# Kernel optimization log

Hardware: AMD Instinct MI355X
Metric: run time of the kernel (lower is better)

The kernel has to match this reference:

```python
import jax, jax.numpy as jnp
import numpy as np

DIM = 1024
HID = 2048
E = 4

def setup_inputs() -> dict:
    key = jax.random.key(0)
    ks = jax.random.split(key, 7)
    s = lambda fan_in: 1.0 / np.sqrt(fan_in)
    x = jax.random.normal(ks[0], (2, 2048, DIM), dtype=jnp.float32)
    W1 = jax.random.uniform(ks[1], (E, DIM, HID), jnp.float32, -s(DIM), s(DIM))
    b1 = jax.random.uniform(ks[2], (E, HID), jnp.float32, -s(DIM), s(DIM))
    W2 = jax.random.uniform(ks[3], (E, HID, DIM), jnp.float32, -s(HID), s(HID))
    b2 = jax.random.uniform(ks[4], (E, DIM), jnp.float32, -s(HID), s(HID))
    Wr = jax.random.uniform(ks[5], (DIM, E), jnp.float32, -s(DIM), s(DIM))
    br = jax.random.uniform(ks[6], (E,), jnp.float32, -s(DIM), s(DIM))
    return {"x": x, "W1": W1, "b1": b1, "W2": W2, "b2": b2, "Wr": Wr, "br": br}

def reference(x, W1, b1, W2, b2, Wr, br):
    # router softmax weights: [B,T,E]
    weights = jax.nn.softmax(x @ Wr + br, axis=-1)
    # all-expert MLP: hidden [B,T,E,H]
    h = jax.nn.gelu(jnp.einsum('btd,edh->bteh', x, W1) + b1, approximate=False)
    # expert outputs [B,T,E,D]
    y = jnp.einsum('bteh,ehd->bted', h, W2) + b2
    # softmax-weighted combine over experts
    return jnp.einsum('bte,bted->btd', weights, y)
```

## Files before the change

### kernel.cpp

```cpp
#include <hip/hip_runtime.h>
#include <hip/hip_bf16.h>
#include <math.h>

#define DIM 1024
#define HID 2048
#define NE  4
#define NT  4096
#define KW  (NE*HID)
#define KSPLIT 2
#define KCH (KW / KSPLIT)

typedef __attribute__((ext_vector_type(8))) short short8;
typedef __attribute__((ext_vector_type(4))) short short4v;
typedef __attribute__((ext_vector_type(4))) float floatx4;


__device__ __forceinline__ void async_cp16(const void* g, void* l) {
  __builtin_amdgcn_global_load_lds(
      (const __attribute__((address_space(1))) void*)g,
      (__attribute__((address_space(3))) void*)l, 16, 0, 0);
}

__device__ __forceinline__ short f2bf(float f) {
  union { float f; unsigned u; } x; x.f = f;
  unsigned r = x.u + 0x7fffu + ((x.u >> 16) & 1u);
  return (short)(r >> 16);
}

__device__ __forceinline__ float gelu_fast(float v) {
  float u = 1.595769122f * (v + 0.044715f * v * v * v);
  return v * __builtin_amdgcn_rcpf(1.0f + __expf(-u));
}

#define VMW(n) asm volatile("s_waitcnt vmcnt(" #n ")" ::: "memory")
#define BAR()  __builtin_amdgcn_s_barrier()

__global__ void router_cvt(const float* __restrict__ x, const float* __restrict__ Wr,
                           const float* __restrict__ br, float* __restrict__ wgt,
                           short* __restrict__ xb) {
  const int wv = threadIdx.x >> 6, lane = threadIdx.x & 63;
  const int t = blockIdx.x * 4 + wv;
  const float* xr = x + (size_t)t * DIM;
  short* xo = xb + (size_t)t * DIM;
  float a0 = 0.f, a1 = 0.f, a2 = 0.f, a3 = 0.f;
  #pragma unroll
  for (int p = 0; p < 4; p++) {
    const int d = p * 256 + lane * 4;
    floatx4 v = *(const floatx4*)&xr[d];
    short4v o;
    #pragma unroll
    for (int j = 0; j < 4; j++) {
      o[j] = f2bf(v[j]);
      floatx4 wr = *(const floatx4*)&Wr[(d + j) * 4];
      a0 += v[j] * wr[0]; a1 += v[j] * wr[1];
      a2 += v[j] * wr[2]; a3 += v[j] * wr[3];
    }
    *(short4v*)&xo[d] = o;
  }
  #pragma unroll
  for (int off = 32; off; off >>= 1) {
    a0 += __shfl_down(a0, off);
    a1 += __shfl_down(a1, off);
    a2 += __shfl_down(a2, off);
    a3 += __shfl_down(a3, off);
  }
  a0 = __shfl(a0, 0); a1 = __shfl(a1, 0); a2 = __shfl(a2, 0); a3 = __shfl(a3, 0);
  float s0 = a0 + br[0], s1 = a1 + br[1], s2 = a2 + br[2], s3 = a3 + br[3];
  float m = fmaxf(fmaxf(s0, s1), fmaxf(s2, s3));
  float e0 = __expf(s0 - m), e1 = __expf(s1 - m), e2 = __expf(s2 - m), e3 = __expf(s3 - m);
  float inv = 1.f / (e0 + e1 + e2 + e3);
  float v = (lane == 0) ? e0 : (lane == 1) ? e1 : (lane == 2) ? e2 : e3;
  if (lane < 4) wgt[t * 4 + lane] = v * inv;
}

#define TP_PADR 136
__global__ void transpose_all(const float* __restrict__ W1, short* __restrict__ w1t,
                              const float* __restrict__ W2, short* __restrict__ w2t) {
  __shared__ __align__(16) short tile[32 * TP_PADR];
  const int b = blockIdx.x;
  const float* in; short* out; int R, C, xt, yt;
  if (b < 2048) {
    const int e = b >> 9, rem = b & 511;
    xt = rem & 63; yt = rem >> 6; R = DIM; C = HID;
    in = W1 + (size_t)e * DIM * HID; out = w1t + (size_t)e * DIM * HID;
  } else {
    const int rem = b - 2048;
    xt = rem & 31; yt = rem >> 5; R = KW; C = DIM;
    in = W2; out = w2t;
  }
  const int c0 = xt * 32, r0 = yt * 128;
  const int t = threadIdx.x;
  const int cin = (t & 7) * 4;
  const int rin = t >> 3;
  #pragma unroll
  for (int i = 0; i < 4; i++) {
    const int r = rin + i * 32;
    floatx4 v = *(const floatx4*)&in[(size_t)(r0 + r) * C + c0 + cin];
    #pragma unroll
    for (int j = 0; j < 4; j++)
      tile[(cin + j) * TP_PADR + r] = f2bf(v[j]);
  }
  __syncthreads();
  const int ct = t >> 3;
  #pragma unroll
  for (int i = 0; i < 2; i++) {
    const int rc = (t & 7) + 8 * i;
    short8 vv = *(const short8*)&tile[ct * TP_PADR + rc * 8];
    *(short8*)&out[(size_t)(c0 + ct) * R + r0 + rc * 8] = vv;
  }
}


__global__ __launch_bounds__(512, 2)
void gemm1_kernel(const short* __restrict__ xb, const short* __restrict__ w1t,
                  const float* __restrict__ b1, const float* __restrict__ wgt,
                  short* __restrict__ hw) {
  __shared__ __align__(16) short lds[65536];
  const int b = blockIdx.x;
  const int xcd = b & 7, slot = b >> 3;
  const int m0 = ((xcd & 3) * 4 + (slot & 3)) * 256;
  const int n0 = ((xcd >> 2) * 16 + (slot >> 2)) * 256;
  const int tid = threadIdx.x;
  const int lane = tid & 63, wv = tid >> 6;
  const int wm = (wv >> 2) * 128, wn = (wv & 3) * 64;
  const int quad = lane >> 4, lrow = lane & 15;

  const int srow = tid >> 3, su = (tid & 7) ^ (srow & 7);
  const int sm = 2 * srow + (su >> 2), skc = su & 3;
  const short* srcA0 = xb + (size_t)(m0 + sm) * DIM + skc * 8;
  const short* srcA1 = srcA0 + (size_t)128 * DIM;
  const short* srcB0 = w1t + (size_t)(n0 + sm) * DIM + skc * 8;
  const short* srcB1 = srcB0 + (size_t)128 * DIM;

  const int cswz = (quad | ((lrow & 1) << 2)) ^ (lrow >> 1);
  const int offA = ((wm >> 1) + (lrow >> 1)) * 64 + cswz * 8;
  const int offB = ((wn >> 1) + (lrow >> 1)) * 64 + cswz * 8;

  floatx4 acc[8][4];
  #pragma unroll
  for (int i = 0; i < 8; i++)
    #pragma unroll
    for (int j = 0; j < 4; j++) acc[i][j] = (floatx4)0.f;

  short8 af[4], bfr[4];

#define G1_SA(sl, tk) do { short* Ab = &lds[(sl) * 8192]; \
    async_cp16(srcA0 + (tk) * 32, Ab + tid * 8); \
    async_cp16(srcA1 + (tk) * 32, Ab + 4096 + tid * 8); } while (0)
#define G1_SB(sl, tk) do { short* Bb = &lds[32768 + (sl) * 8192]; \
    async_cp16(srcB0 + (tk) * 32, Bb + tid * 8); \
    async_cp16(srcB1 + (tk) * 32, Bb + 4096 + tid * 8); } while (0)

#define G1_PH0(sl) do { \
    const short* Ab = &lds[(sl) * 8192]; const short* Bb = &lds[32768 + (sl) * 8192]; \
    _Pragma("unroll") for (int j = 0; j < 4; j++) \
      bfr[j] = *(const short8*)&Bb[offB + j * 512]; \
    _Pragma("unroll") for (int i = 0; i < 4; i++) \
      af[i] = *(const short8*)&Ab[offA + i * 512]; \
    __builtin_amdgcn_s_setprio(1); \
    _Pragma("unroll") for (int i = 0; i < 4; i++) \
      _Pragma("unroll") for (int j = 0; j < 4; j++) \
        acc[i][j] = __builtin_amdgcn_mfma_f32_16x16x32_bf16(af[i], bfr[j], acc[i][j], 0, 0, 0); \
    __builtin_amdgcn_s_setprio(0); } while (0)
#define G1_PH1(sl) do { \
    const short* Ab = &lds[(sl) * 8192]; \
    _Pragma("unroll") for (int i = 0; i < 4; i++) \
      af[i] = *(const short8*)&Ab[offA + (4 + i) * 512]; \
    __builtin_amdgcn_s_setprio(1); \
    _Pragma("unroll") for (int i = 0; i < 4; i++) \
      _Pragma("unroll") for (int j = 0; j < 4; j++) \
        acc[4 + i][j] = __builtin_amdgcn_mfma_f32_16x16x32_bf16(af[i], bfr[j], acc[4 + i][j], 0, 0, 0); \
    __builtin_amdgcn_s_setprio(0); } while (0)

  G1_SA(0, 0); G1_SB(0, 0); G1_SA(1, 1); G1_SB(1, 1);
  for (int t = 0; t < 28; t += 4) {
    G1_SA(2, t + 2); VMW(6); BAR(); G1_PH0(0); G1_SB(2, t + 2); G1_PH1(0);
    G1_SA(3, t + 3); VMW(6); BAR(); G1_PH0(1); G1_SB(3, t + 3); G1_PH1(1);
    G1_SA(0, t + 4); VMW(6); BAR(); G1_PH0(2); G1_SB(0, t + 4); G1_PH1(2);
    G1_SA(1, t + 5); VMW(6); BAR(); G1_PH0(3); G1_SB(1, t + 5); G1_PH1(3);
  }
  G1_SA(2, 30); VMW(6); BAR(); G1_PH0(0); G1_SB(2, 30); G1_PH1(0);
  G1_SA(3, 31); VMW(6); BAR(); G1_PH0(1); G1_SB(3, 31); G1_PH1(1);
  VMW(4); BAR(); G1_PH0(2); G1_PH1(2);
  VMW(0); BAR(); G1_PH0(3); G1_PH1(3);
#undef G1_SA
#undef G1_SB
#undef G1_PH0
#undef G1_PH1

  const int e = n0 >> 11;
  #pragma unroll
  for (int i = 0; i < 8; i++) {
    const int rbase = m0 + wm + i * 16 + quad * 4;
    float w4[4];
    #pragma unroll
    for (int r = 0; r < 4; r++) w4[r] = wgt[(rbase + r) * NE + e];
    #pragma unroll
    for (int j = 0; j < 4; j++) {
      const int col = n0 + wn + j * 16 + lrow;
      const float b1v = b1[e * HID + (col & (HID - 1))];
      #pragma unroll
      for (int r = 0; r < 4; r++) {
        float v = acc[i][j][r] + b1v;
        hw[(size_t)(rbase + r) * KW + col] = f2bf(w4[r] * gelu_fast(v));
      }
    }
  }
}

__global__ __launch_bounds__(512, 2)
void gemm2_kernel(const short* __restrict__ hw, const short* __restrict__ w2t,
                  const float* __restrict__ b2, const float* __restrict__ wgt,
                  float* __restrict__ out, float* __restrict__ part) {
  __shared__ __align__(16) short lds[49152];
  const int b = blockIdx.x;
  const int xcd = b & 7, slot = b >> 3;
  const int kz = xcd >> 2;
  const int m0 = ((xcd & 3) * 4 + (slot & 3)) * 256;
  const int n0 = (slot >> 2) * 128;
  const int tid = threadIdx.x;
  const int lane = tid & 63, wv = tid >> 6;
  const int wm = (wv >> 1) * 64, wn = (wv & 1) * 64;
  const int quad = lane >> 4, lrow = lane & 15;

  const int srow = tid >> 3, su = (tid & 7) ^ (srow & 7);
  const int sm = 2 * srow + (su >> 2), skc = su & 3;
  const short* srcA0 = hw + (size_t)(m0 + sm) * KW + kz * KCH + skc * 8;
  const short* srcA1 = srcA0 + (size_t)128 * KW;
  const short* srcB0 = w2t + (size_t)(n0 + sm) * KW + kz * KCH + skc * 8;

  const int cswz = (quad | ((lrow & 1) << 2)) ^ (lrow >> 1);
  const int offA = ((wm >> 1) + (lrow >> 1)) * 64 + cswz * 8;
  const int offB = ((wn >> 1) + (lrow >> 1)) * 64 + cswz * 8;

  floatx4 acc[4][4];
  #pragma unroll
  for (int i = 0; i < 4; i++)
    #pragma unroll
    for (int j = 0; j < 4; j++) acc[i][j] = (floatx4)0.f;

  short8 af[2], bfr[4];

#define G2_SA(sl, tk) do { short* Ab = &lds[(sl) * 8192]; \
    async_cp16(srcA0 + (tk) * 32, Ab + tid * 8); \
    async_cp16(srcA1 + (tk) * 32, Ab + 4096 + tid * 8); } while (0)
#define G2_SB(sl, tk) do { short* Bb = &lds[32768 + (sl) * 4096]; \
    async_cp16(srcB0 + (tk) * 32, Bb + tid * 8); } while (0)

#define G2_PH0(sl) do { \
    const short* Ab = &lds[(sl) * 8192]; const short* Bb = &lds[32768 + (sl) * 4096]; \
    _Pragma("unroll") for (int j = 0; j < 4; j++) \
      bfr[j] = *(const short8*)&Bb[offB + j * 512]; \
    _Pragma("unroll") for (int i = 0; i < 2; i++) \
      af[i] = *(const short8*)&Ab[offA + i * 512]; \
    __builtin_amdgcn_s_setprio(1); \
    _Pragma("unroll") for (int i = 0; i < 2; i++) \
      _Pragma("unroll") for (int j = 0; j < 4; j++) \
        acc[i][j] = __builtin_amdgcn_mfma_f32_16x16x32_bf16(af[i], bfr[j], acc[i][j], 0, 0, 0); \
    __builtin_amdgcn_s_setprio(0); } while (0)
#define G2_PH1(sl) do { \
    const short* Ab = &lds[(sl) * 8192]; \
    _Pragma("unroll") for (int i = 0; i < 2; i++) \
      af[i] = *(const short8*)&Ab[offA + (2 + i) * 512]; \
    __builtin_amdgcn_s_setprio(1); \
    _Pragma("unroll") for (int i = 0; i < 2; i++) \
      _Pragma("unroll") for (int j = 0; j < 4; j++) \
        acc[2 + i][j] = __builtin_amdgcn_mfma_f32_16x16x32_bf16(af[i], bfr[j], acc[2 + i][j], 0, 0, 0); \
    __builtin_amdgcn_s_setprio(0); } while (0)

  G2_SA(0, 0); G2_SB(0, 0); G2_SA(1, 1); G2_SB(1, 1);
  for (int t = 0; t < 124; t += 4) {
    G2_SA(2, t + 2); VMW(5); BAR(); G2_PH0(0); G2_SB(2, t + 2); G2_PH1(0);
    G2_SA(3, t + 3); VMW(5); BAR(); G2_PH0(1); G2_SB(3, t + 3); G2_PH1(1);
    G2_SA(0, t + 4); VMW(5); BAR(); G2_PH0(2); G2_SB(0, t + 4); G2_PH1(2);
    G2_SA(1, t + 5); VMW(5); BAR(); G2_PH0(3); G2_SB(1, t + 5); G2_PH1(3);
  }
  G2_SA(2, 126); VMW(5); BAR(); G2_PH0(0); G2_SB(2, 126); G2_PH1(0);
  G2_SA(3, 127); VMW(5); BAR(); G2_PH0(1); G2_SB(3, 127); G2_PH1(1);
  VMW(3); BAR(); G2_PH0(2); G2_PH1(2);
  VMW(0); BAR(); G2_PH0(3); G2_PH1(3);
#undef G2_SA
#undef G2_SB
#undef G2_PH0
#undef G2_PH1

  if (kz == 0) {
    #pragma unroll
    for (int i = 0; i < 4; i++) {
      const int rbase = m0 + wm + i * 16 + quad * 4;
      floatx4 wr[4];
      #pragma unroll
      for (int r = 0; r < 4; r++) wr[r] = *(const floatx4*)&wgt[(rbase + r) * NE];
      #pragma unroll
      for (int j = 0; j < 4; j++) {
        const int col = n0 + wn + j * 16 + lrow;
        float b2v[4];
        #pragma unroll
        for (int eI = 0; eI < 4; eI++) b2v[eI] = b2[eI * DIM + col];
        #pragma unroll
        for (int r = 0; r < 4; r++) {
          float bias = wr[r][0] * b2v[0] + wr[r][1] * b2v[1] +
                       wr[r][2] * b2v[2] + wr[r][3] * b2v[3];
          out[(size_t)(rbase + r) * DIM + col] = acc[i][j][r] + bias;
        }
      }
    }
  } else {
    #pragma unroll
    for (int i = 0; i < 4; i++) {
      const int rbase = m0 + wm + i * 16 + quad * 4;
      #pragma unroll
      for (int j = 0; j < 4; j++) {
        const int col = n0 + wn + j * 16 + lrow;
        #pragma unroll
        for (int r = 0; r < 4; r++)
          part[(size_t)(rbase + r) * DIM + col] = acc[i][j][r];
      }
    }
  }
}

__global__ void reduce_out(float* __restrict__ out, const float* __restrict__ part) {
  int i = (blockIdx.x * 256 + threadIdx.x) * 4;
  floatx4 v = *(const floatx4*)&out[i];
  floatx4 a = *(const floatx4*)&part[i];
  v = v + a;
  *(floatx4*)&out[i] = v;
}


extern "C" void kernel_launch(void* const* d_in, const int* in_sizes, int n_in,
                              void* d_out, int out_size, void* d_ws, size_t ws_size,
                              hipStream_t stream) {
  const float* x  = (const float*)d_in[0];
  const float* W1 = (const float*)d_in[1];
  const float* b1 = (const float*)d_in[2];
  const float* W2 = (const float*)d_in[3];
  const float* b2 = (const float*)d_in[4];
  const float* Wr = (const float*)d_in[5];
  const float* br = (const float*)d_in[6];
  float* out = (float*)d_out;

  char* ws = (char*)d_ws;
  float* wgt = (float*)(ws);
  short* w2t = (short*)(ws + 65536);
  short* hw  = (short*)(ws + 65536 + 16777216);
  short* xb  = (short*)(ws + 65536 + 16777216 + 67108864);
  short* w1t = (short*)(ws + 65536 + 16777216 + 67108864 + 8388608);
  float* part= (float*)(ws + 65536 + 16777216 + 67108864);

  hipLaunchKernelGGL(router_cvt, dim3(NT / 4), dim3(256), 0, stream, x, Wr, br, wgt, xb);
  hipLaunchKernelGGL(transpose_all, dim3(2048 + 2048), dim3(256), 0, stream,
                     W1, w1t, W2, w2t);
  hipLaunchKernelGGL(gemm1_kernel, dim3(512), dim3(512), 0, stream,
                     xb, w1t, b1, wgt, hw);
  hipLaunchKernelGGL(gemm2_kernel, dim3(256), dim3(512), 0, stream,
                     hw, w2t, b2, wgt, out, part);
  hipLaunchKernelGGL(reduce_out, dim3(NT * DIM / 1024), dim3(256), 0, stream, out, part);
}
```

Baseline: 278.9 us.

## Merge router and transpose kernels; restructure GEMM main loops with barrier-split LDS reads

The router/bf16-convert kernel and the weight-transpose kernel are merged into one prep kernel, with the first 1024 blocks doing routing, which removes one launch and gap. Both GEMM main loops are reorganised so that LDS fragment reads are issued before the async global-to-LDS copies. Explicit lgkmcnt waits and extra barriers now separate the reads from the MFMA phases, replacing the earlier prefetch-distance scheduling. The aim is cleaner overlap of the LDS reads with the copies into other slots, at the price of twice as many barriers per k-step.

```diff
diff --git a/kernel.cpp b/kernel.cpp
--- a/kernel.cpp
+++ b/kernel.cpp
@@ -32,52 +32,54 @@
   return v * __builtin_amdgcn_rcpf(1.0f + __expf(-u));
 }
 
-#define VMW(n) asm volatile("s_waitcnt vmcnt(" #n ")" ::: "memory")
-#define BAR()  __builtin_amdgcn_s_barrier()
-
-__global__ void router_cvt(const float* __restrict__ x, const float* __restrict__ Wr,
-                           const float* __restrict__ br, float* __restrict__ wgt,
-                           short* __restrict__ xb) {
-  const int wv = threadIdx.x >> 6, lane = threadIdx.x & 63;
-  const int t = blockIdx.x * 4 + wv;
-  const float* xr = x + (size_t)t * DIM;
-  short* xo = xb + (size_t)t * DIM;
-  float a0 = 0.f, a1 = 0.f, a2 = 0.f, a3 = 0.f;
-  #pragma unroll
-  for (int p = 0; p < 4; p++) {
-    const int d = p * 256 + lane * 4;
-    floatx4 v = *(const floatx4*)&xr[d];
-    short4v o;
-    #pragma unroll
-    for (int j = 0; j < 4; j++) {
-      o[j] = f2bf(v[j]);
-      floatx4 wr = *(const floatx4*)&Wr[(d + j) * 4];
-      a0 += v[j] * wr[0]; a1 += v[j] * wr[1];
-      a2 += v[j] * wr[2]; a3 += v[j] * wr[3];
-    }
-    *(short4v*)&xo[d] = o;
-  }
-  #pragma unroll
-  for (int off = 32; off; off >>= 1) {
-    a0 += __shfl_down(a0, off);
-    a1 += __shfl_down(a1, off);
-    a2 += __shfl_down(a2, off);
-    a3 += __shfl_down(a3, off);
-  }
-  a0 = __shfl(a0, 0); a1 = __shfl(a1, 0); a2 = __shfl(a2, 0); a3 = __shfl(a3, 0);
-  float s0 = a0 + br[0], s1 = a1 + br[1], s2 = a2 + br[2], s3 = a3 + br[3];
-  float m = fmaxf(fmaxf(s0, s1), fmaxf(s2, s3));
-  float e0 = __expf(s0 - m), e1 = __expf(s1 - m), e2 = __expf(s2 - m), e3 = __expf(s3 - m);
-  float inv = 1.f / (e0 + e1 + e2 + e3);
-  float v = (lane == 0) ? e0 : (lane == 1) ? e1 : (lane == 2) ? e2 : e3;
-  if (lane < 4) wgt[t * 4 + lane] = v * inv;
-}
+#define VMW(n)  asm volatile("s_waitcnt vmcnt(" #n ")" ::: "memory")
+#define LGKM0() asm volatile("s_waitcnt lgkmcnt(0)" ::: "memory")
+#define BAR()   __builtin_amdgcn_s_barrier()
 
 #define TP_PADR 136
-__global__ void transpose_all(const float* __restrict__ W1, short* __restrict__ w1t,
-                              const float* __restrict__ W2, short* __restrict__ w2t) {
+__global__ void prep_kernel(const float* __restrict__ x, const float* __restrict__ Wr,
+                            const float* __restrict__ br, float* __restrict__ wgt,
+                            short* __restrict__ xb,
+                            const float* __restrict__ W1, short* __restrict__ w1t,
+                            const float* __restrict__ W2, short* __restrict__ w2t) {
   __shared__ __align__(16) short tile[32 * TP_PADR];
-  const int b = blockIdx.x;
+  if (blockIdx.x < 1024) {
+    const int wv = threadIdx.x >> 6, lane = threadIdx.x & 63;
+    const int t = blockIdx.x * 4 + wv;
+    const float* xr = x + (size_t)t * DIM;
+    short* xo = xb + (size_t)t * DIM;
+    float a0 = 0.f, a1 = 0.f, a2 = 0.f, a3 = 0.f;
+    #pragma unroll
+    for (int p = 0; p < 4; p++) {
+      const int d = p * 256 + lane * 4;
+      floatx4 v = *(const floatx4*)&xr[d];
+      short4v o;
+      #pragma unroll
+      for (int j = 0; j < 4; j++) {
+        o[j] = f2bf(v[j]);
+        floatx4 wr = *(const floatx4*)&Wr[(d + j) * 4];
+        a0 += v[j] * wr[0]; a1 += v[j] * wr[1];
+        a2 += v[j] * wr[2]; a3 += v[j] * wr[3];
+      }
+      *(short4v*)&xo[d] = o;
+    }
+    #pragma unroll
+    for (int off = 32; off; off >>= 1) {
+      a0 += __shfl_down(a0, off);
+      a1 += __shfl_down(a1, off);
+      a2 += __shfl_down(a2, off);
+      a3 += __shfl_down(a3, off);
+    }
+    a0 = __shfl(a0, 0); a1 = __shfl(a1, 0); a2 = __shfl(a2, 0); a3 = __shfl(a3, 0);
+    float s0 = a0 + br[0], s1 = a1 + br[1], s2 = a2 + br[2], s3 = a3 + br[3];
+    float m = fmaxf(fmaxf(s0, s1), fmaxf(s2, s3));
+    float e0 = __expf(s0 - m), e1 = __expf(s1 - m), e2 = __expf(s2 - m), e3 = __expf(s3 - m);
+    float inv = 1.f / (e0 + e1 + e2 + e3);
+    float v = (lane == 0) ? e0 : (lane == 1) ? e1 : (lane == 2) ? e2 : e3;
+    if (lane < 4) wgt[t * 4 + lane] = v * inv;
+    return;
+  }
+  const int b = blockIdx.x - 1024;
   const float* in; short* out; int R, C, xt, yt;
   if (b < 2048) {
     const int e = b >> 9, rem = b & 511;
@@ -144,49 +146,62 @@
 
   short8 af[4], bfr[4];
 
-#define G1_SA(sl, tk) do { short* Ab = &lds[(sl) * 8192]; \
-    async_cp16(srcA0 + (tk) * 32, Ab + tid * 8); \
-    async_cp16(srcA1 + (tk) * 32, Ab + 4096 + tid * 8); } while (0)
-#define G1_SB(sl, tk) do { short* Bb = &lds[32768 + (sl) * 8192]; \
-    async_cp16(srcB0 + (tk) * 32, Bb + tid * 8); \
-    async_cp16(srcB1 + (tk) * 32, Bb + 4096 + tid * 8); } while (0)
-
-#define G1_PH0(sl) do { \
-    const short* Ab = &lds[(sl) * 8192]; const short* Bb = &lds[32768 + (sl) * 8192]; \
+#define G1_SA(tk) do { short* Aw = &lds[((tk) & 3) * 8192]; \
+    async_cp16(srcA0 + (size_t)(tk) * 32, Aw + tid * 8); \
+    async_cp16(srcA1 + (size_t)(tk) * 32, Aw + 4096 + tid * 8); } while (0)
+#define G1_SB(tk) do { short* Bw = &lds[32768 + ((tk) & 3) * 8192]; \
+    async_cp16(srcB0 + (size_t)(tk) * 32, Bw + tid * 8); \
+    async_cp16(srcB1 + (size_t)(tk) * 32, Bw + 4096 + tid * 8); } while (0)
+#define G1_RD0(sl) do { \
     _Pragma("unroll") for (int j = 0; j < 4; j++) \
-      bfr[j] = *(const short8*)&Bb[offB + j * 512]; \
+      bfr[j] = *(const short8*)&lds[32768 + (sl) * 8192 + offB + j * 512]; \
     _Pragma("unroll") for (int i = 0; i < 4; i++) \
-      af[i] = *(const short8*)&Ab[offA + i * 512]; \
-    __builtin_amdgcn_s_setprio(1); \
+      af[i] = *(const short8*)&lds[(sl) * 8192 + offA + i * 512]; } while (0)
+#define G1_RD1(sl) do { \
+    _Pragma("unroll") for (int i = 0; i < 4; i++) \
+      af[i] = *(const short8*)&lds[(sl) * 8192 + offA + (4 + i) * 512]; } while (0)
+#define G1_MM0 do { __builtin_amdgcn_s_setprio(1); \
     _Pragma("unroll") for (int i = 0; i < 4; i++) \
       _Pragma("unroll") for (int j = 0; j < 4; j++) \
         acc[i][j] = __builtin_amdgcn_mfma_f32_16x16x32_bf16(af[i], bfr[j], acc[i][j], 0, 0, 0); \
     __builtin_amdgcn_s_setprio(0); } while (0)
-#define G1_PH1(sl) do { \
-    const short* Ab = &lds[(sl) * 8192]; \
-    _Pragma("unroll") for (int i = 0; i < 4; i++) \
-      af[i] = *(const short8*)&Ab[offA + (4 + i) * 512]; \
-    __builtin_amdgcn_s_setprio(1); \
+#define G1_MM1 do { __builtin_amdgcn_s_setprio(1); \
     _Pragma("unroll") for (int i = 0; i < 4; i++) \
       _Pragma("unroll") for (int j = 0; j < 4; j++) \
         acc[4 + i][j] = __builtin_amdgcn_mfma_f32_16x16x32_bf16(af[i], bfr[j], acc[4 + i][j], 0, 0, 0); \
     __builtin_amdgcn_s_setprio(0); } while (0)
 
-  G1_SA(0, 0); G1_SB(0, 0); G1_SA(1, 1); G1_SB(1, 1);
+#define G1_STEP(sl, tk) do { \
+    G1_RD0(sl); G1_SA(tk); BAR(); LGKM0(); G1_MM0; BAR(); \
+    G1_RD1(sl); G1_SB(tk); VMW(4); BAR(); LGKM0(); G1_MM1; BAR(); } while (0)
+#define G1_STEP_V0(sl) do { \
+    G1_RD0(sl); BAR(); LGKM0(); G1_MM0; BAR(); \
+    G1_RD1(sl); VMW(0); BAR(); LGKM0(); G1_MM1; BAR(); } while (0)
+#define G1_STEP_END(sl) do { \
+    G1_RD0(sl); BAR(); LGKM0(); G1_MM0; BAR(); \
+    G1_RD1(sl); LGKM0(); G1_MM1; } while (0)
+
+  G1_SA(0); G1_SB(0); G1_SA(1); G1_SB(1);
+  VMW(4); BAR();
   for (int t = 0; t < 28; t += 4) {
-    G1_SA(2, t + 2); VMW(6); BAR(); G1_PH0(0); G1_SB(2, t + 2); G1_PH1(0);
-    G1_SA(3, t + 3); VMW(6); BAR(); G1_PH0(1); G1_SB(3, t + 3); G1_PH1(1);
-    G1_SA(0, t + 4); VMW(6); BAR(); G1_PH0(2); G1_SB(0, t + 4); G1_PH1(2);
-    G1_SA(1, t + 5); VMW(6); BAR(); G1_PH0(3); G1_SB(1, t + 5); G1_PH1(3);
-  }
-  G1_SA(2, 30); VMW(6); BAR(); G1_PH0(0); G1_SB(2, 30); G1_PH1(0);
-  G1_SA(3, 31); VMW(6); BAR(); G1_PH0(1); G1_SB(3, 31); G1_PH1(1);
-  VMW(4); BAR(); G1_PH0(2); G1_PH1(2);
-  VMW(0); BAR(); G1_PH0(3); G1_PH1(3);
+    G1_STEP(0, t + 2);
+    G1_STEP(1, t + 3);
+    G1_STEP(2, t + 4);
+    G1_STEP(3, t + 5);
+  }
+  G1_STEP(0, 30);
+  G1_STEP(1, 31);
+  G1_STEP_V0(2);
+  G1_STEP_END(3);
 #undef G1_SA
 #undef G1_SB
-#undef G1_PH0
-#undef G1_PH1
+#undef G1_RD0
+#undef G1_RD1
+#undef G1_MM0
+#undef G1_MM1
+#undef G1_STEP
+#undef G1_STEP_V0
+#undef G1_STEP_END
 
   const int e = n0 >> 11;
   #pragma unroll
@@ -241,48 +256,61 @@
 
   short8 af[2], bfr[4];
 
-#define G2_SA(sl, tk) do { short* Ab = &lds[(sl) * 8192]; \
-    async_cp16(srcA0 + (tk) * 32, Ab + tid * 8); \
-    async_cp16(srcA1 + (tk) * 32, Ab + 4096 + tid * 8); } while (0)
-#define G2_SB(sl, tk) do { short* Bb = &lds[32768 + (sl) * 4096]; \
-    async_cp16(srcB0 + (tk) * 32, Bb + tid * 8); } while (0)
-
-#define G2_PH0(sl) do { \
-    const short* Ab = &lds[(sl) * 8192]; const short* Bb = &lds[32768 + (sl) * 4096]; \
+#define G2_SA(tk) do { short* Aw = &lds[((tk) & 3) * 8192]; \
+    async_cp16(srcA0 + (size_t)(tk) * 32, Aw + tid * 8); \
+    async_cp16(srcA1 + (size_t)(tk) * 32, Aw + 4096 + tid * 8); } while (0)
+#define G2_SB(tk) do { short* Bw = &lds[32768 + ((tk) & 3) * 4096]; \
+    async_cp16(srcB0 + (size_t)(tk) * 32, Bw + tid * 8); } while (0)
+#define G2_RD0(sl) do { \
     _Pragma("unroll") for (int j = 0; j < 4; j++) \
-      bfr[j] = *(const short8*)&Bb[offB + j * 512]; \
+      bfr[j] = *(const short8*)&lds[32768 + (sl) * 4096 + offB + j * 512]; \
     _Pragma("unroll") for (int i = 0; i < 2; i++) \
-      af[i] = *(const short8*)&Ab[offA + i * 512]; \
-    __builtin_amdgcn_s_setprio(1); \
+      af[i] = *(const short8*)&lds[(sl) * 8192 + offA + i * 512]; } while (0)
+#define G2_RD1(sl) do { \
+    _Pragma("unroll") for (int i = 0; i < 2; i++) \
+      af[i] = *(const short8*)&lds[(sl) * 8192 + offA + (2 + i) * 512]; } while (0)
+#define G2_MM0 do { __builtin_amdgcn_s_setprio(1); \
     _Pragma("unroll") for (int i = 0; i < 2; i++) \
       _Pragma("unroll") for (int j = 0; j < 4; j++) \
         acc[i][j] = __builtin_amdgcn_mfma_f32_16x16x32_bf16(af[i], bfr[j], acc[i][j], 0, 0, 0); \
     __builtin_amdgcn_s_setprio(0); } while (0)
-#define G2_PH1(sl) do { \
-    const short* Ab = &lds[(sl) * 8192]; \
-    _Pragma("unroll") for (int i = 0; i < 2; i++) \
-      af[i] = *(const short8*)&Ab[offA + (2 + i) * 512]; \
-    __builtin_amdgcn_s_setprio(1); \
+#define G2_MM1 do { __builtin_amdgcn_s_setprio(1); \
     _Pragma("unroll") for (int i = 0; i < 2; i++) \
       _Pragma("unroll") for (int j = 0; j < 4; j++) \
         acc[2 + i][j] = __builtin_amdgcn_mfma_f32_16x16x32_bf16(af[i], bfr[j], acc[2 + i][j], 0, 0, 0); \
     __builtin_amdgcn_s_setprio(0); } while (0)
 
-  G2_SA(0, 0); G2_SB(0, 0); G2_SA(1, 1); G2_SB(1, 1);
+#define G2_STEP(sl, tk) do { \
+    G2_RD0(sl); G2_SA(tk); BAR(); LGKM0(); G2_MM0; BAR(); \
+    G2_RD1(sl); G2_SB(tk); VMW(3); BAR(); LGKM0(); G2_MM1; BAR(); } while (0)
+#define G2_STEP_V0(sl) do { \
+    G2_RD0(sl); BAR(); LGKM0(); G2_MM0; BAR(); \
+    G2_RD1(sl); VMW(0); BAR(); LGKM0(); G2_MM1; BAR(); } while (0)
+#define G2_STEP_END(sl) do { \
+    G2_RD0(sl); BAR(); LGKM0(); G2_MM0; BAR(); \
+    G2_RD1(sl); LGKM0(); G2_MM1; } while (0)
+
+  G2_SA(0); G2_SB(0); G2_SA(1); G2_SB(1);
+  VMW(3); BAR();
   for (int t = 0; t < 124; t += 4) {
-    G2_SA(2, t + 2); VMW(5); BAR(); G2_PH0(0); G2_SB(2, t + 2); G2_PH1(0);
-    G2_SA(3, t + 3); VMW(5); BAR(); G2_PH0(1); G2_SB(3, t + 3); G2_PH1(1);
-    G2_SA(0, t + 4); VMW(5); BAR(); G2_PH0(2); G2_SB(0, t + 4); G2_PH1(2);
-    G2_SA(1, t + 5); VMW(5); BAR(); G2_PH0(3); G2_SB(1, t + 5); G2_PH1(3);
-  }
-  G2_SA(2, 126); VMW(5); BAR(); G2_PH0(0); G2_SB(2, 126); G2_PH1(0);
-  G2_SA(3, 127); VMW(5); BAR(); G2_PH0(1); G2_SB(3, 127); G2_PH1(1);
-  VMW(3); BAR(); G2_PH0(2); G2_PH1(2);
-  VMW(0); BAR(); G2_PH0(3); G2_PH1(3);
+    G2_STEP(0, t + 2);
+    G2_STEP(1, t + 3);
+    G2_STEP(2, t + 4);
+    G2_STEP(3, t + 5);
+  }
+  G2_STEP(0, 126);
+  G2_STEP(1, 127);
+  G2_STEP_V0(2);
+  G2_STEP_END(3);
 #undef G2_SA
 #undef G2_SB
-#undef G2_PH0
-#undef G2_PH1
+#undef G2_RD0
+#undef G2_RD1
+#undef G2_MM0
+#undef G2_MM1
+#undef G2_STEP
+#undef G2_STEP_V0
+#undef G2_STEP_END
 
   if (kz == 0) {
     #pragma unroll
@@ -349,9 +377,8 @@
   short* w1t = (short*)(ws + 65536 + 16777216 + 67108864 + 8388608);
   float* part= (float*)(ws + 65536 + 16777216 + 67108864);
 
-  hipLaunchKernelGGL(router_cvt, dim3(NT / 4), dim3(256), 0, stream, x, Wr, br, wgt, xb);
-  hipLaunchKernelGGL(transpose_all, dim3(2048 + 2048), dim3(256), 0, stream,
-                     W1, w1t, W2, w2t);
+  hipLaunchKernelGGL(prep_kernel, dim3(1024 + 4096), dim3(256), 0, stream,
+                     x, Wr, br, wgt, xb, W1, w1t, W2, w2t);
   hipLaunchKernelGGL(gemm1_kernel, dim3(512), dim3(512), 0, stream,
                      xb, w1t, b1, wgt, hw);
   hipLaunchKernelGGL(gemm2_kernel, dim3(256), dim3(512), 0, stream,
```

New measurement: 280.5 us. About the same (+0.6%).

## Switch both GEMMs to 32x32x16 MFMA tiles and merge prep kernels

Applied to the files above, without the earlier changes.

Both GEMM kernels now use the 32x32x16 bf16 MFMA instruction with 16-wide accumulators instead of 16x16x32, which changes the LDS fragment addressing, the swizzle and the epilogue row mapping. Larger MFMA tiles mean fewer LDS fragment reads per FLOP and fewer instructions to issue. The router/convert kernel and the weight transpose kernel are also merged into one launch to save a kernel boundary. The risk is more register pressure from the larger accumulators, and the new epilogue writes are less contiguous.

```diff
diff --git a/kernel.cpp b/kernel.cpp
--- a/kernel.cpp
+++ b/kernel.cpp
@@ -13,6 +13,7 @@
 typedef __attribute__((ext_vector_type(8))) short short8;
 typedef __attribute__((ext_vector_type(4))) short short4v;
 typedef __attribute__((ext_vector_type(4))) float floatx4;
+typedef __attribute__((ext_vector_type(16))) float floatx16;
 
 
 __device__ __forceinline__ void async_cp16(const void* g, void* l) {
@@ -35,49 +36,51 @@
 #define VMW(n) asm volatile("s_waitcnt vmcnt(" #n ")" ::: "memory")
 #define BAR()  __builtin_amdgcn_s_barrier()
 
-__global__ void router_cvt(const float* __restrict__ x, const float* __restrict__ Wr,
-                           const float* __restrict__ br, float* __restrict__ wgt,
-                           short* __restrict__ xb) {
-  const int wv = threadIdx.x >> 6, lane = threadIdx.x & 63;
-  const int t = blockIdx.x * 4 + wv;
-  const float* xr = x + (size_t)t * DIM;
-  short* xo = xb + (size_t)t * DIM;
-  float a0 = 0.f, a1 = 0.f, a2 = 0.f, a3 = 0.f;
-  #pragma unroll
-  for (int p = 0; p < 4; p++) {
-    const int d = p * 256 + lane * 4;
-    floatx4 v = *(const floatx4*)&xr[d];
-    short4v o;
-    #pragma unroll
-    for (int j = 0; j < 4; j++) {
-      o[j] = f2bf(v[j]);
-      floatx4 wr = *(const floatx4*)&Wr[(d + j) * 4];
-      a0 += v[j] * wr[0]; a1 += v[j] * wr[1];
-      a2 += v[j] * wr[2]; a3 += v[j] * wr[3];
-    }
-    *(short4v*)&xo[d] = o;
-  }
-  #pragma unroll
-  for (int off = 32; off; off >>= 1) {
-    a0 += __shfl_down(a0, off);
-    a1 += __shfl_down(a1, off);
-    a2 += __shfl_down(a2, off);
-    a3 += __shfl_down(a3, off);
-  }
-  a0 = __shfl(a0, 0); a1 = __shfl(a1, 0); a2 = __shfl(a2, 0); a3 = __shfl(a3, 0);
-  float s0 = a0 + br[0], s1 = a1 + br[1], s2 = a2 + br[2], s3 = a3 + br[3];
-  float m = fmaxf(fmaxf(s0, s1), fmaxf(s2, s3));
-  float e0 = __expf(s0 - m), e1 = __expf(s1 - m), e2 = __expf(s2 - m), e3 = __expf(s3 - m);
-  float inv = 1.f / (e0 + e1 + e2 + e3);
-  float v = (lane == 0) ? e0 : (lane == 1) ? e1 : (lane == 2) ? e2 : e3;
-  if (lane < 4) wgt[t * 4 + lane] = v * inv;
-}
-
 #define TP_PADR 136
-__global__ void transpose_all(const float* __restrict__ W1, short* __restrict__ w1t,
-                              const float* __restrict__ W2, short* __restrict__ w2t) {
+
+__global__ void prep_kernel(const float* __restrict__ x, const float* __restrict__ Wr,
+                            const float* __restrict__ br, float* __restrict__ wgt,
+                            short* __restrict__ xb,
+                            const float* __restrict__ W1, short* __restrict__ w1t,
+                            const float* __restrict__ W2, short* __restrict__ w2t) {
   __shared__ __align__(16) short tile[32 * TP_PADR];
-  const int b = blockIdx.x;
+  if (blockIdx.x < 1024) {
+    const int wv = threadIdx.x >> 6, lane = threadIdx.x & 63;
+    const int t = blockIdx.x * 4 + wv;
+    const float* xr = x + (size_t)t * DIM;
+    short* xo = xb + (size_t)t * DIM;
+    float a0 = 0.f, a1 = 0.f, a2 = 0.f, a3 = 0.f;
+    #pragma unroll
+    for (int p = 0; p < 4; p++) {
+      const int d = p * 256 + lane * 4;
+      floatx4 v = *(const floatx4*)&xr[d];
+      short4v o;
+      #pragma unroll
+      for (int j = 0; j < 4; j++) {
+        o[j] = f2bf(v[j]);
+        floatx4 wr = *(const floatx4*)&Wr[(d + j) * 4];
+        a0 += v[j] * wr[0]; a1 += v[j] * wr[1];
+        a2 += v[j] * wr[2]; a3 += v[j] * wr[3];
+      }
+      *(short4v*)&xo[d] = o;
+    }
+    #pragma unroll
+    for (int off = 32; off; off >>= 1) {
+      a0 += __shfl_down(a0, off);
+      a1 += __shfl_down(a1, off);
+      a2 += __shfl_down(a2, off);
+      a3 += __shfl_down(a3, off);
+    }
+    a0 = __shfl(a0, 0); a1 = __shfl(a1, 0); a2 = __shfl(a2, 0); a3 = __shfl(a3, 0);
+    float s0 = a0 + br[0], s1 = a1 + br[1], s2 = a2 + br[2], s3 = a3 + br[3];
+    float m = fmaxf(fmaxf(s0, s1), fmaxf(s2, s3));
+    float e0 = __expf(s0 - m), e1 = __expf(s1 - m), e2 = __expf(s2 - m), e3 = __expf(s3 - m);
+    float inv = 1.f / (e0 + e1 + e2 + e3);
+    float v = (lane == 0) ? e0 : (lane == 1) ? e1 : (lane == 2) ? e2 : e3;
+    if (lane < 4) wgt[t * 4 + lane] = v * inv;
+    return;
+  }
+  const int b = blockIdx.x - 1024;
   const float* in; short* out; int R, C, xt, yt;
   if (b < 2048) {
     const int e = b >> 9, rem = b & 511;
@@ -123,7 +126,7 @@
   const int tid = threadIdx.x;
   const int lane = tid & 63, wv = tid >> 6;
   const int wm = (wv >> 2) * 128, wn = (wv & 3) * 64;
-  const int quad = lane >> 4, lrow = lane & 15;
+  const int l31 = lane & 31, hi = lane >> 5;
 
   const int srow = tid >> 3, su = (tid & 7) ^ (srow & 7);
   const int sm = 2 * srow + (su >> 2), skc = su & 3;
@@ -132,44 +135,50 @@
   const short* srcB0 = w1t + (size_t)(n0 + sm) * DIM + skc * 8;
   const short* srcB1 = srcB0 + (size_t)128 * DIM;
 
-  const int cswz = (quad | ((lrow & 1) << 2)) ^ (lrow >> 1);
-  const int offA = ((wm >> 1) + (lrow >> 1)) * 64 + cswz * 8;
-  const int offB = ((wn >> 1) + (lrow >> 1)) * 64 + cswz * 8;
-
-  floatx4 acc[8][4];
-  #pragma unroll
-  for (int i = 0; i < 8; i++)
-    #pragma unroll
-    for (int j = 0; j < 4; j++) acc[i][j] = (floatx4)0.f;
-
-  short8 af[4], bfr[4];
+  const int rsw = (l31 >> 1) & 7;
+  const int cK0 = (((l31 & 1) << 2) | hi) ^ rsw;
+  const int cK1 = (((l31 & 1) << 2) | (2 + hi)) ^ rsw;
+  const int rowA = (wm >> 1) + (l31 >> 1);
+  const int rowB = (wn >> 1) + (l31 >> 1);
+  const int offA0 = rowA * 64 + cK0 * 8, offA1 = rowA * 64 + cK1 * 8;
+  const int offB0 = rowB * 64 + cK0 * 8, offB1 = rowB * 64 + cK1 * 8;
+
+  floatx16 acc[4][2];
+  #pragma unroll
+  for (int i = 0; i < 4; i++)
+    #pragma unroll
+    for (int j = 0; j < 2; j++) acc[i][j] = (floatx16)0.f;
+
+  short8 af[4], bfr[2];
 
 #define G1_SA(sl, tk) do { short* Ab = &lds[(sl) * 8192]; \
-    async_cp16(srcA0 + (tk) * 32, Ab + tid * 8); \
-    async_cp16(srcA1 + (tk) * 32, Ab + 4096 + tid * 8); } while (0)
+    async_cp16(srcA0 + (size_t)(tk) * 32, Ab + tid * 8); \
+    async_cp16(srcA1 + (size_t)(tk) * 32, Ab + 4096 + tid * 8); } while (0)
 #define G1_SB(sl, tk) do { short* Bb = &lds[32768 + (sl) * 8192]; \
-    async_cp16(srcB0 + (tk) * 32, Bb + tid * 8); \
-    async_cp16(srcB1 + (tk) * 32, Bb + 4096 + tid * 8); } while (0)
+    async_cp16(srcB0 + (size_t)(tk) * 32, Bb + tid * 8); \
+    async_cp16(srcB1 + (size_t)(tk) * 32, Bb + 4096 + tid * 8); } while (0)
 
 #define G1_PH0(sl) do { \
     const short* Ab = &lds[(sl) * 8192]; const short* Bb = &lds[32768 + (sl) * 8192]; \
-    _Pragma("unroll") for (int j = 0; j < 4; j++) \
-      bfr[j] = *(const short8*)&Bb[offB + j * 512]; \
+    _Pragma("unroll") for (int j = 0; j < 2; j++) \
+      bfr[j] = *(const short8*)&Bb[offB0 + j * 1024]; \
     _Pragma("unroll") for (int i = 0; i < 4; i++) \
-      af[i] = *(const short8*)&Ab[offA + i * 512]; \
+      af[i] = *(const short8*)&Ab[offA0 + i * 1024]; \
     __builtin_amdgcn_s_setprio(1); \
     _Pragma("unroll") for (int i = 0; i < 4; i++) \
-      _Pragma("unroll") for (int j = 0; j < 4; j++) \
-        acc[i][j] = __builtin_amdgcn_mfma_f32_16x16x32_bf16(af[i], bfr[j], acc[i][j], 0, 0, 0); \
+      _Pragma("unroll") for (int j = 0; j < 2; j++) \
+        acc[i][j] = __builtin_amdgcn_mfma_f32_32x32x16_bf16(af[i], bfr[j], acc[i][j], 0, 0, 0); \
     __builtin_amdgcn_s_setprio(0); } while (0)
 #define G1_PH1(sl) do { \
-    const short* Ab = &lds[(sl) * 8192]; \
+    const short* Ab = &lds[(sl) * 8192]; const short* Bb = &lds[32768 + (sl) * 8192]; \
+    _Pragma("unroll") for (int j = 0; j < 2; j++) \
+      bfr[j] = *(const short8*)&Bb[offB1 + j * 1024]; \
     _Pragma("unroll") for (int i = 0; i < 4; i++) \
-      af[i] = *(const short8*)&Ab[offA + (4 + i) * 512]; \
+      af[i] = *(const short8*)&Ab[offA1 + i * 1024]; \
     __builtin_amdgcn_s_setprio(1); \
     _Pragma("unroll") for (int i = 0; i < 4; i++) \
-      _Pragma("unroll") for (int j = 0; j < 4; j++) \
-        acc[4 + i][j] = __builtin_amdgcn_mfma_f32_16x16x32_bf16(af[i], bfr[j], acc[4 + i][j], 0, 0, 0); \
+      _Pragma("unroll") for (int j = 0; j < 2; j++) \
+        acc[i][j] = __builtin_amdgcn_mfma_f32_32x32x16_bf16(af[i], bfr[j], acc[i][j], 0, 0, 0); \
     __builtin_amdgcn_s_setprio(0); } while (0)
 
   G1_SA(0, 0); G1_SB(0, 0); G1_SA(1, 1); G1_SB(1, 1);
@@ -189,20 +198,20 @@
 #undef G1_PH1
 
   const int e = n0 >> 11;
-  #pragma unroll
-  for (int i = 0; i < 8; i++) {
-    const int rbase = m0 + wm + i * 16 + quad * 4;
-    float w4[4];
-    #pragma unroll
-    for (int r = 0; r < 4; r++) w4[r] = wgt[(rbase + r) * NE + e];
-    #pragma unroll
-    for (int j = 0; j < 4; j++) {
-      const int col = n0 + wn + j * 16 + lrow;
-      const float b1v = b1[e * HID + (col & (HID - 1))];
-      #pragma unroll
-      for (int r = 0; r < 4; r++) {
-        float v = acc[i][j][r] + b1v;
-        hw[(size_t)(rbase + r) * KW + col] = f2bf(w4[r] * gelu_fast(v));
+  float b1v[2];
+  #pragma unroll
+  for (int j = 0; j < 2; j++)
+    b1v[j] = b1[e * HID + ((n0 + wn + j * 32 + l31) & (HID - 1))];
+  #pragma unroll
+  for (int i = 0; i < 4; i++) {
+    #pragma unroll
+    for (int r = 0; r < 16; r++) {
+      const int R = m0 + wm + i * 32 + (r & 3) + 8 * (r >> 2) + 4 * hi;
+      const float w = wgt[R * NE + e];
+      #pragma unroll
+      for (int j = 0; j < 2; j++) {
+        const int col = n0 + wn + j * 32 + l31;
+        hw[(size_t)R * KW + col] = f2bf(w * gelu_fast(acc[i][j][r] + b1v[j]));
       }
     }
   }
@@ -221,7 +230,7 @@
   const int tid = threadIdx.x;
   const int lane = tid & 63, wv = tid >> 6;
   const int wm = (wv >> 1) * 64, wn = (wv & 1) * 64;
-  const int quad = lane >> 4, lrow = lane & 15;
+  const int l31 = lane & 31, hi = lane >> 5;
 
   const int srow = tid >> 3, su = (tid & 7) ^ (srow & 7);
   const int sm = 2 * srow + (su >> 2), skc = su & 3;
@@ -229,43 +238,49 @@
   const short* srcA1 = srcA0 + (size_t)128 * KW;
   const short* srcB0 = w2t + (size_t)(n0 + sm) * KW + kz * KCH + skc * 8;
 
-  const int cswz = (quad | ((lrow & 1) << 2)) ^ (lrow >> 1);
-  const int offA = ((wm >> 1) + (lrow >> 1)) * 64 + cswz * 8;
-  const int offB = ((wn >> 1) + (lrow >> 1)) * 64 + cswz * 8;
-
-  floatx4 acc[4][4];
-  #pragma unroll
-  for (int i = 0; i < 4; i++)
-    #pragma unroll
-    for (int j = 0; j < 4; j++) acc[i][j] = (floatx4)0.f;
-
-  short8 af[2], bfr[4];
+  const int rsw = (l31 >> 1) & 7;
+  const int cK0 = (((l31 & 1) << 2) | hi) ^ rsw;
+  const int cK1 = (((l31 & 1) << 2) | (2 + hi)) ^ rsw;
+  const int rowA = (wm >> 1) + (l31 >> 1);
+  const int rowB = (wn >> 1) + (l31 >> 1);
+  const int offA0 = rowA * 64 + cK0 * 8, offA1 = rowA * 64 + cK1 * 8;
+  const int offB0 = rowB * 64 + cK0 * 8, offB1 = rowB * 64 + cK1 * 8;
+
+  floatx16 acc[2][2];
+  #pragma unroll
+  for (int i = 0; i < 2; i++)
+    #pragma unroll
+    for (int j = 0; j < 2; j++) acc[i][j] = (floatx16)0.f;
+
+  short8 af[2], bfr[2];
 
 #define G2_SA(sl, tk) do { short* Ab = &lds[(sl) * 8192]; \
-    async_cp16(srcA0 + (tk) * 32, Ab + tid * 8); \
-    async_cp16(srcA1 + (tk) * 32, Ab + 4096 + tid * 8); } while (0)
+    async_cp16(srcA0 + (size_t)(tk) * 32, Ab + tid * 8); \
+    async_cp16(srcA1 + (size_t)(tk) * 32, Ab + 4096 + tid * 8); } while (0)
 #define G2_SB(sl, tk) do { short* Bb = &lds[32768 + (sl) * 4096]; \
-    async_cp16(srcB0 + (tk) * 32, Bb + tid * 8); } while (0)
+    async_cp16(srcB0 + (size_t)(tk) * 32, Bb + tid * 8); } while (0)
 
 #define G2_PH0(sl) do { \
     const short* Ab = &lds[(sl) * 8192]; const short* Bb = &lds[32768 + (sl) * 4096]; \
-    _Pragma("unroll") for (int j = 0; j < 4; j++) \
-      bfr[j] = *(const short8*)&Bb[offB + j * 512]; \
+    _Pragma("unroll") for (int j = 0; j < 2; j++) \
+      bfr[j] = *(const short8*)&Bb[offB0 + j * 1024]; \
     _Pragma("unroll") for (int i = 0; i < 2; i++) \
-      af[i] = *(const short8*)&Ab[offA + i * 512]; \
+      af[i] = *(const short8*)&Ab[offA0 + i * 1024]; \
     __builtin_amdgcn_s_setprio(1); \
     _Pragma("unroll") for (int i = 0; i < 2; i++) \
-      _Pragma("unroll") for (int j = 0; j < 4; j++) \
-        acc[i][j] = __builtin_amdgcn_mfma_f32_16x16x32_bf16(af[i], bfr[j], acc[i][j], 0, 0, 0); \
+      _Pragma("unroll") for (int j = 0; j < 2; j++) \
+        acc[i][j] = __builtin_amdgcn_mfma_f32_32x32x16_bf16(af[i], bfr[j], acc[i][j], 0, 0, 0); \
     __builtin_amdgcn_s_setprio(0); } while (0)
 #define G2_PH1(sl) do { \
-    const short* Ab = &lds[(sl) * 8192]; \
+    const short* Ab = &lds[(sl) * 8192]; const short* Bb = &lds[32768 + (sl) * 4096]; \
+    _Pragma("unroll") for (int j = 0; j < 2; j++) \
+      bfr[j] = *(const short8*)&Bb[offB1 + j * 1024]; \
     _Pragma("unroll") for (int i = 0; i < 2; i++) \
-      af[i] = *(const short8*)&Ab[offA + (2 + i) * 512]; \
+      af[i] = *(const short8*)&Ab[offA1 + i * 1024]; \
     __builtin_amdgcn_s_setprio(1); \
     _Pragma("unroll") for (int i = 0; i < 2; i++) \
-      _Pragma("unroll") for (int j = 0; j < 4; j++) \
-        acc[2 + i][j] = __builtin_amdgcn_mfma_f32_16x16x32_bf16(af[i], bfr[j], acc[2 + i][j], 0, 0, 0); \
+      _Pragma("unroll") for (int j = 0; j < 2; j++) \
+        acc[i][j] = __builtin_amdgcn_mfma_f32_32x32x16_bf16(af[i], bfr[j], acc[i][j], 0, 0, 0); \
     __builtin_amdgcn_s_setprio(0); } while (0)
 
   G2_SA(0, 0); G2_SB(0, 0); G2_SA(1, 1); G2_SB(1, 1);
@@ -285,36 +300,39 @@
 #undef G2_PH1
 
   if (kz == 0) {
-    #pragma unroll
-    for (int i = 0; i < 4; i++) {
-      const int rbase = m0 + wm + i * 16 + quad * 4;
-      floatx4 wr[4];
-      #pragma unroll
-      for (int r = 0; r < 4; r++) wr[r] = *(const floatx4*)&wgt[(rbase + r) * NE];
-      #pragma unroll
-      for (int j = 0; j < 4; j++) {
-        const int col = n0 + wn + j * 16 + lrow;
-        float b2v[4];
+    float b2v[2][4];
+    #pragma unroll
+    for (int j = 0; j < 2; j++) {
+      const int col = n0 + wn + j * 32 + l31;
+      #pragma unroll
+      for (int eI = 0; eI < 4; eI++) b2v[j][eI] = b2[eI * DIM + col];
+    }
+    #pragma unroll
+    for (int i = 0; i < 2; i++) {
+      #pragma unroll
+      for (int r = 0; r < 16; r++) {
+        const int R = m0 + wm + i * 32 + (r & 3) + 8 * (r >> 2) + 4 * hi;
+        floatx4 wr = *(const floatx4*)&wgt[R * NE];
         #pragma unroll
-        for (int eI = 0; eI < 4; eI++) b2v[eI] = b2[eI * DIM + col];
-        #pragma unroll
-        for (int r = 0; r < 4; r++) {
-          float bias = wr[r][0] * b2v[0] + wr[r][1] * b2v[1] +
-                       wr[r][2] * b2v[2] + wr[r][3] * b2v[3];
-          out[(size_t)(rbase + r) * DIM + col] = acc[i][j][r] + bias;
+        for (int j = 0; j < 2; j++) {
+          const int col = n0 + wn + j * 32 + l31;
+          float bias = wr[0] * b2v[j][0] + wr[1] * b2v[j][1] +
+                       wr[2] * b2v[j][2] + wr[3] * b2v[j][3];
+          out[(size_t)R * DIM + col] = acc[i][j][r] + bias;
         }
       }
     }
   } else {
     #pragma unroll
-    for (int i = 0; i < 4; i++) {
-      const int rbase = m0 + wm + i * 16 + quad * 4;
-      #pragma unroll
-      for (int j = 0; j < 4; j++) {
-        const int col = n0 + wn + j * 16 + lrow;
+    for (int i = 0; i < 2; i++) {
+      #pragma unroll
+      for (int r = 0; r < 16; r++) {
+        const int R = m0 + wm + i * 32 + (r & 3) + 8 * (r >> 2) + 4 * hi;
         #pragma unroll
-        for (int r = 0; r < 4; r++)
-          part[(size_t)(rbase + r) * DIM + col] = acc[i][j][r];
+        for (int j = 0; j < 2; j++) {
+          const int col = n0 + wn + j * 32 + l31;
+          part[(size_t)R * DIM + col] = acc[i][j][r];
+        }
       }
     }
   }
@@ -349,9 +367,8 @@
   short* w1t = (short*)(ws + 65536 + 16777216 + 67108864 + 8388608);
   float* part= (float*)(ws + 65536 + 16777216 + 67108864);
 
-  hipLaunchKernelGGL(router_cvt, dim3(NT / 4), dim3(256), 0, stream, x, Wr, br, wgt, xb);
-  hipLaunchKernelGGL(transpose_all, dim3(2048 + 2048), dim3(256), 0, stream,
-                     W1, w1t, W2, w2t);
+  hipLaunchKernelGGL(prep_kernel, dim3(1024 + 2048 + 2048), dim3(256), 0, stream,
+                     x, Wr, br, wgt, xb, W1, w1t, W2, w2t);
   hipLaunchKernelGGL(gemm1_kernel, dim3(512), dim3(512), 0, stream,
                      xb, w1t, b1, wgt, hw);
   hipLaunchKernelGGL(gemm2_kernel, dim3(256), dim3(512), 0, stream,
```

Result: no change. 282.5 us (+1.3%).
